# Optimization experiments

Measured on AMD Instinct MI355X. Metric: run time of the kernel, lower is better.

## Reference

```python
import jax, jax.numpy as jnp
import numpy as np

B, M, D = 16, 16, 512          # m (tokens per sample) must equal num_experts
N = 16                          # num_experts
H = (D + D) * 2 // 3            # hidden_dim = 682
OUT = 512


def setup_inputs() -> dict:
    key = jax.random.key(0)
    ks = jax.random.split(key, 8)
    s = lambda k, shape, fan: jax.random.normal(k, shape, jnp.float32) / np.sqrt(fan)
    return {
        "x":    jax.random.normal(ks[0], (B, M, D), jnp.float32),
        "phi":  jax.random.normal(ks[1], (D, N, H), jnp.float32),
        "W1":   s(ks[2], (N, D, H), D),
        "b1":   s(ks[3], (N, H), D),
        "W2":   s(ks[4], (N, H, D), H),
        "b2":   s(ks[5], (N, D), H),
        "Wout": s(ks[6], (N * D, OUT), N * D),
        "bout": s(ks[7], (OUT,), N * D),
    }


def reference(x, phi, W1, b1, W2, b2, Wout, bout):
    # dispatch/combine logits: [b, m, n, p]
    logits = jnp.einsum('bmd,dnp->bmnp', x, phi)
    Dw = jax.nn.softmax(logits, axis=1)                       # dispatch weights over tokens m
    Cw = jax.nn.softmax(jax.nn.softmax(logits, axis=2), axis=3)  # (softmax of softmax, faithful)
    Xs = jnp.einsum('bmd,bmnp->bnpd', x, Dw)                  # expert slot inputs [b,n,p,d]
    # batched per-expert MLP (grouped GEMM over expert axis n)
    hmid = jax.nn.relu(jnp.einsum('bnpd,ndh->bnph', Xs, W1) + b1[None, :, None, :])
    Ys = jnp.einsum('bnph,nhd->bnpd', hmid, W2) + b2[None, :, None, :]
    Y = jnp.einsum('bnpd,bmnp->bmd', Ys, Cw)                  # combine -> [b, m, d]
    flat = Y.reshape(Y.shape[0], -1)                          # [b, m*d] == [b, n*d]
    return flat @ Wout + bout
```

## Files before the change

### kernel.cpp

```cpp
#include <hip/hip_runtime.h>
#include <hip/hip_bf16.h>
#include <math.h>

typedef unsigned int   u32;
typedef unsigned short u16;
typedef __bf16 bf16;
typedef bf16  bf16x8  __attribute__((ext_vector_type(8)));
typedef float f32x4   __attribute__((ext_vector_type(4)));
typedef float f32x16  __attribute__((ext_vector_type(16)));

#define BBATCH 16
#define MTOK   16
#define NEXP   16
#define DDIM   512
#define HDIM   682
#define HPAD   704
#define NHCOL  (NEXP*HDIM)
#define NHPCOL (NEXP*HPAD)

__device__ __forceinline__ u16 f2bf(float f) {
    u32 u = __builtin_bit_cast(u32, f);
    u += 0x7fffu + ((u >> 16) & 1u);
    return (u16)(u >> 16);
}
__device__ __forceinline__ float bf2f(u16 h) {
    u32 u = ((u32)h) << 16;
    return __builtin_bit_cast(float, u);
}
__device__ __forceinline__ u32 pk2bf(float a, float b) {
    __hip_bfloat162 t = __float22bfloat162_rn(float2{a, b});
    u32 r;
    __builtin_memcpy(&r, &t, 4);
    return r;
}

__global__ __launch_bounds__(256) void k_prep(
    const float* __restrict__ x, const float* __restrict__ b2,
    const float* __restrict__ bout,
    u16* __restrict__ xh, u16* __restrict__ xl,
    float* __restrict__ Y, float* __restrict__ out, u16* __restrict__ DwT) {
    const int bid = blockIdx.x, tid = threadIdx.x;
    if (bid < 128) {
        int i = (bid * 256 + tid) * 4;
        float4 v = *(const float4*)&x[i];
        float a[4] = {v.x, v.y, v.z, v.w};
        u16 hh[4], ll[4];
        #pragma unroll
        for (int j = 0; j < 4; ++j) {
            hh[j] = f2bf(a[j]);
            ll[j] = f2bf(a[j] - bf2f(hh[j]));
        }
        *(uint2*)&xh[i] = make_uint2((u32)hh[0] | ((u32)hh[1] << 16), (u32)hh[2] | ((u32)hh[3] << 16));
        *(uint2*)&xl[i] = make_uint2((u32)ll[0] | ((u32)ll[1] << 16), (u32)ll[2] | ((u32)ll[3] << 16));
    } else if (bid < 640) {
        int idx = (bid - 128) * 256 + tid;
        int d = idx & 511;
        float s = 0.f;
        #pragma unroll
        for (int nn = 0; nn < 16; ++nn) s += b2[nn * 512 + d];
        Y[idx] = s;
    } else if (bid < 672) {
        int idx = (bid - 640) * 256 + tid;
        out[idx] = bout[idx & 511];
    } else {
        int g = (bid - 672) * 256 + tid;
        int bn = g / 88, off = g - bn * 88;
        *(uint2*)(DwT + (size_t)(bn * HPAD + HDIM) * 16 + off * 4) = make_uint2(0u, 0u);
    }
}

__global__ __launch_bounds__(256) void k_lt1(
    const u16* __restrict__ xh, const u16* __restrict__ xl,
    const float* __restrict__ phi, const float* __restrict__ W1,
    float* __restrict__ logits, u16* __restrict__ DwT, u16* __restrict__ T1b) {
    __shared__ __align__(16) char SMEM[29184];
    const int bid = blockIdx.x, tid = threadIdx.x;
    const int wv = tid >> 6, lane = tid & 63, quad = lane >> 4, l15 = lane & 15;
    if (bid < 704) {
        const int xcd = bid & 7, slot = bid >> 3;
        const int rt = slot & 3, ct = (slot >> 2) * 8 + xcd;
        if (ct >= 171) return;
        u16* AH = (u16*)SMEM;
        u16* AL = (u16*)(SMEM + 5120);
        u16* BH = (u16*)(SMEM + 10240);
        u16* BL = (u16*)(SMEM + 15360);
        float* F = (float*)(SMEM + 20480);
        const int r = tid >> 2, kg = (tid & 3) * 8;
        const u16* aph = xh + (size_t)(rt * 64 + r) * 512 + kg;
        const u16* apl = xl + (size_t)(rt * 64 + r) * 512 + kg;
        const int dl = tid >> 3, cg = (tid & 7) * 8;
        const int c0 = ct * 64 + cg;
        float vB[8];
        auto loadB = [&](int kb) {
            const float* src = phi + (size_t)(kb + dl) * NHCOL + c0;
            if (c0 + 8 <= NHCOL) {
                *(float4*)&vB[0] = *(const float4*)&src[0];
                *(float4*)&vB[4] = *(const float4*)&src[4];
            } else {
                #pragma unroll
                for (int i = 0; i < 8; ++i) vB[i] = (c0 + i < NHCOL) ? src[i] : 0.f;
            }
        };
        uint4 rAh = *(const uint4*)aph;
        uint4 rAl = *(const uint4*)apl;
        loadB(0);
        f32x4 acc[4] = {};
        for (int kb = 0; kb < 512; kb += 32) {
            *(uint4*)&AH[r * 40 + kg] = rAh;
            *(uint4*)&AL[r * 40 + kg] = rAl;
            *(float4*)&F[dl * 68 + cg]     = *(float4*)&vB[0];
            *(float4*)&F[dl * 68 + cg + 4] = *(float4*)&vB[4];
            __syncthreads();
            if (kb + 32 < 512) {
                rAh = *(const uint4*)(aph + kb + 32);
                rAl = *(const uint4*)(apl + kb + 32);
                loadB(kb + 32);
            }
            {
                int cc = tid & 63, q = tid >> 6;
                u16 th[8], tl[8];
                #pragma unroll
                for (int i = 0; i < 8; ++i) {
                    float v = F[(q * 8 + i) * 68 + cc];
                    th[i] = f2bf(v);
                    tl[i] = f2bf(v - bf2f(th[i]));
                }
                *(uint4*)&BH[cc * 40 + q * 8] = *(uint4*)&th[0];
                *(uint4*)&BL[cc * 40 + q * 8] = *(uint4*)&tl[0];
            }
            __syncthreads();
            bf16x8 ah = *(const bf16x8*)&AH[(wv * 16 + l15) * 40 + quad * 8];
            bf16x8 al = *(const bf16x8*)&AL[(wv * 16 + l15) * 40 + quad * 8];
            #pragma unroll
            for (int j = 0; j < 4; ++j) {
                bf16x8 bh = *(const bf16x8*)&BH[(j * 16 + l15) * 40 + quad * 8];
                bf16x8 bl = *(const bf16x8*)&BL[(j * 16 + l15) * 40 + quad * 8];
                acc[j] = __builtin_amdgcn_mfma_f32_16x16x32_bf16(ah, bh, acc[j], 0, 0, 0);
                acc[j] = __builtin_amdgcn_mfma_f32_16x16x32_bf16(ah, bl, acc[j], 0, 0, 0);
                acc[j] = __builtin_amdgcn_mfma_f32_16x16x32_bf16(al, bh, acc[j], 0, 0, 0);
            }
            __syncthreads();
        }
        const int b  = rt * 4 + wv;
        const int r0 = rt * 64 + wv * 16 + quad * 4;
        #pragma unroll
        for (int j = 0; j < 4; ++j) {
            const int col = ct * 64 + j * 16 + l15;
            float a0 = acc[j][0], a1 = acc[j][1], a2 = acc[j][2], a3 = acc[j][3];
            if (col < NHCOL) {
                logits[(size_t)(r0 + 0) * NHCOL + col] = a0;
                logits[(size_t)(r0 + 1) * NHCOL + col] = a1;
                logits[(size_t)(r0 + 2) * NHCOL + col] = a2;
                logits[(size_t)(r0 + 3) * NHCOL + col] = a3;
            }
            float mx = fmaxf(fmaxf(a0, a1), fmaxf(a2, a3));
            mx = fmaxf(mx, __shfl_xor(mx, 16));
            mx = fmaxf(mx, __shfl_xor(mx, 32));
            float e0 = expf(a0 - mx), e1 = expf(a1 - mx);
            float e2 = expf(a2 - mx), e3 = expf(a3 - mx);
            float s = e0 + e1 + e2 + e3;
            s += __shfl_xor(s, 16);
            s += __shfl_xor(s, 32);
            float inv = 1.f / s;
            if (col < NHCOL) {
                int n = col / HDIM;
                int p = col - n * HDIM;
                u16* dst = DwT + ((size_t)((b * 16 + n) * HPAD + p)) * 16 + quad * 4;
                *(uint2*)dst = make_uint2(pk2bf(e0 * inv, e1 * inv), pk2bf(e2 * inv, e3 * inv));
            }
        }
    } else {
        const int b2_ = bid - 704;
        const int xcd = b2_ & 7, slot = b2_ >> 3;
        const int rh = slot & 1, ct = (slot >> 1) * 8 + xcd;
        const int n = ct / 11, h0 = (ct % 11) * 64;
        u16* As = (u16*)SMEM;
        u16* Bs = (u16*)(SMEM + 10240);
        float* F = (float*)(SMEM + 15360);
        const int r = tid >> 1, kg = (tid & 1) * 16;
        const u16* ap = xh + (size_t)(rh * 128 + r) * 512 + kg;
        const int dl = tid >> 3, cg = (tid & 7) * 8;
        const int h = h0 + cg;
        float vB[8];
        auto loadB = [&](int kb) {
            const float* wr = W1 + ((size_t)n * 512 + kb + dl) * HDIM + h;
            if (h + 8 <= HDIM) {
                #pragma unroll
                for (int i = 0; i < 4; ++i) {
                    float2 t = *(const float2*)&wr[i * 2];
                    vB[i * 2] = t.x; vB[i * 2 + 1] = t.y;
                }
            } else {
                #pragma unroll
                for (int i = 0; i < 8; ++i) vB[i] = (h + i < HDIM) ? wr[i] : 0.f;
            }
        };
        uint4 rA0 = *(const uint4*)ap;
        uint4 rA1 = *(const uint4*)(ap + 8);
        loadB(0);
        f32x4 acc[2][4] = {};
        for (int kb = 0; kb < 512; kb += 32) {
            *(uint4*)&As[r * 40 + kg]     = rA0;
            *(uint4*)&As[r * 40 + kg + 8] = rA1;
            *(float4*)&F[dl * 68 + cg]     = *(float4*)&vB[0];
            *(float4*)&F[dl * 68 + cg + 4] = *(float4*)&vB[4];
            __syncthreads();
            if (kb + 32 < 512) {
                rA0 = *(const uint4*)(ap + kb + 32);
                rA1 = *(const uint4*)(ap + kb + 40);
                loadB(kb + 32);
            }
            {
                int cc = tid & 63, q = tid >> 6;
                u16 tv[8];
                #pragma unroll
                for (int i = 0; i < 8; ++i) tv[i] = f2bf(F[(q * 8 + i) * 68 + cc]);
                *(uint4*)&Bs[cc * 40 + q * 8] = *(uint4*)&tv[0];
            }
            __syncthreads();
            bf16x8 af[2], bfr[4];
            #pragma unroll
            for (int i = 0; i < 2; ++i)
                af[i] = *(const bf16x8*)&As[(wv * 32 + i * 16 + l15) * 40 + quad * 8];
            #pragma unroll
            for (int j = 0; j < 4; ++j)
                bfr[j] = *(const bf16x8*)&Bs[(j * 16 + l15) * 40 + quad * 8];
            #pragma unroll
            for (int i = 0; i < 2; ++i)
                #pragma unroll
                for (int j = 0; j < 4; ++j)
                    acc[i][j] = __builtin_amdgcn_mfma_f32_16x16x32_bf16(af[i], bfr[j], acc[i][j], 0, 0, 0);
            __syncthreads();
        }
        #pragma unroll
        for (int i = 0; i < 2; ++i)
            #pragma unroll
            for (int j = 0; j < 4; ++j) {
                int col = ct * 64 + j * 16 + l15;
                int r0  = rh * 128 + wv * 32 + i * 16 + quad * 4;
                #pragma unroll
                for (int rr = 0; rr < 4; ++rr)
                    T1b[(size_t)(r0 + rr) * NHPCOL + col] = f2bf(acc[i][j][rr]);
            }
    }
}

__global__ __launch_bounds__(256) void k_cw(
    const float* __restrict__ L, u16* __restrict__ CwB) {
    __shared__ float row[NHCOL];
    const int bid = blockIdx.x, tid = threadIdx.x;
    const int m = bid & 15, b = bid >> 4;
    const float* Lrow = L + (size_t)(b * 16 + m) * NHCOL;
    for (int i = tid; i < NHCOL; i += 256) row[i] = Lrow[i];
    __syncthreads();
    for (int p = tid; p < HDIM; p += 256) {
        float v[16];
        float mx = -1e30f;
        #pragma unroll
        for (int n = 0; n < 16; ++n) { v[n] = row[n * HDIM + p]; mx = fmaxf(mx, v[n]); }
        float s = 0.f;
        #pragma unroll
        for (int n = 0; n < 16; ++n) { v[n] = expf(v[n] - mx); s += v[n]; }
        float inv = 1.f / s;
        #pragma unroll
        for (int n = 0; n < 16; ++n) row[n * HDIM + p] = expf(v[n] * inv);
    }
    __syncthreads();
    const int wv = tid >> 6, lane = tid & 63;
    for (int nn = 0; nn < 4; ++nn) {
        int n = wv * 4 + nn;
        float s = 0.f;
        for (int p = lane; p < HDIM; p += 64) s += row[n * HDIM + p];
        #pragma unroll
        for (int off = 32; off > 0; off >>= 1) s += __shfl_xor(s, off);
        float inv = 1.f / s;
        u16* dst = CwB + (size_t)(((b * 16 + n) * 16 + m)) * HPAD;
        for (int p = lane; p < HDIM; p += 64) dst[p] = f2bf(row[n * HDIM + p] * inv);
        if (lane < HPAD - HDIM) dst[HDIM + lane] = 0;
    }
}

__global__ __launch_bounds__(256) void k_mid(
    const u16* __restrict__ T1b, const u16* __restrict__ DwT,
    const u16* __restrict__ CwB, const float* __restrict__ b1,
    u16* __restrict__ Gb) {
    __shared__ u16 T1T[128 * 24];
    __shared__ u16 hmidT[128 * 64];
    const int bid = blockIdx.x;
    const int xcd = bid & 7, slot = bid >> 3;
    const int ht = slot % 6, gg = slot / 6;
    const int g = gg * 8 + xcd;
    const int n = g & 15, b = g >> 4;
    const int tid = threadIdx.x;
    const int wv = tid >> 6, lane = tid & 63;
    const int quad = lane >> 4, l15 = lane & 15;
    const int l31 = lane & 31, half = lane >> 5;
    const int h0 = ht * 128;
    const int b16n = b * 16 + n;

    {
        int m = tid & 15, hh0 = (tid >> 4) * 8;
        u16 v[8];
        if (h0 + hh0 + 8 <= HPAD) {
            *(uint4*)v = *(const uint4*)(T1b + (size_t)(b * 16 + m) * NHPCOL + n * HPAD + h0 + hh0);
        } else {
            #pragma unroll
            for (int i = 0; i < 8; ++i) v[i] = 0;
        }
        #pragma unroll
        for (int i = 0; i < 8; ++i) T1T[(hh0 + i) * 24 + m] = v[i];
    }
    __syncthreads();

    const int hrow = wv * 32 + l31;
    bf16x8 bt1 = *(const bf16x8*)&T1T[hrow * 24 + half * 8];
    int hg1 = h0 + hrow;
    float biasf = (hg1 < HDIM) ? b1[n * HDIM + hg1] : 0.f;
    f32x16 cbias;
    #pragma unroll
    for (int i = 0; i < 16; ++i) cbias[i] = biasf;

    const u16* dwbase = DwT + (size_t)(b16n * HPAD) * 16;
    const u16* cwrow  = CwB + (size_t)(b16n * 16 + l15) * HPAD;

    f32x4 acc[2] = {};
    const int hsw = hrow & 7;
    for (int c = 0; c < 11; ++c) {
        const int p0 = c * 64;
        #pragma unroll
        for (int pt = 0; pt < 2; ++pt) {
            bf16x8 adw = *(const bf16x8*)(dwbase + (size_t)(p0 + pt * 32 + l31) * 16 + half * 8);
            f32x16 hm = __builtin_amdgcn_mfma_f32_32x32x16_bf16(adw, bt1, cbias, 0, 0, 0);
            #pragma unroll
            for (int g2 = 0; g2 < 4; ++g2) {
                float v0 = fmaxf(hm[g2 * 4 + 0], 0.f);
                float v1 = fmaxf(hm[g2 * 4 + 1], 0.f);
                float v2 = fmaxf(hm[g2 * 4 + 2], 0.f);
                float v3 = fmaxf(hm[g2 * 4 + 3], 0.f);
                uint2 pk = make_uint2(pk2bf(v0, v1), pk2bf(v2, v3));
                int gran = (pt * 4 + g2) ^ hsw;
                *(uint2*)&hmidT[hrow * 64 + gran * 8 + half * 4] = pk;
            }
        }
        #pragma unroll
        for (int s = 0; s < 2; ++s) {
            bf16x8 acw = *(const bf16x8*)(cwrow + p0 + s * 32 + quad * 8);
            #pragma unroll
            for (int hj = 0; hj < 2; ++hj) {
                int hr = wv * 32 + hj * 16 + l15;
                int gr = (s * 4 + quad) ^ (hr & 7);
                bf16x8 bh = *(const bf16x8*)&hmidT[hr * 64 + gr * 8];
                acc[hj] = __builtin_amdgcn_mfma_f32_16x16x32_bf16(acw, bh, acc[hj], 0, 0, 0);
            }
        }
    }
    #pragma unroll
    for (int hj = 0; hj < 2; ++hj) {
        int h = h0 + wv * 32 + hj * 16 + l15;
        if (h < HPAD) {
            #pragma unroll
            for (int r = 0; r < 4; ++r) {
                int m = quad * 4 + r;
                Gb[(size_t)(b * 16 + m) * NHPCOL + n * HPAD + h] = f2bf(acc[hj][r]);
            }
        }
    }
}

__global__ __launch_bounds__(256) void k_ygemm(
    const u16* __restrict__ G, const float* __restrict__ W2, float* __restrict__ Y) {
    __shared__ u16 AsL[64 * 40];
    __shared__ u16 BsL[128 * 40];
    __shared__ float F[32 * 132];
    const int bid = blockIdx.x;
    const int xcd = bid & 7, slot = bid >> 3;
    const int rt = slot & 3, gg = slot >> 2;
    const int g = gg * 8 + xcd;
    const int ct = g & 3, nz = g >> 2;
    const int n = nz >> 1, kb0 = (nz & 1) * 352;
    const int tid = threadIdx.x;
    const int wv = tid >> 6, lane = tid & 63, quad = lane >> 4, l15 = lane & 15;
    const int m0 = rt * 64, d0 = ct * 128;
    const int am = tid >> 2, akg = (tid & 3) * 8;
    const u16* apg = G + (size_t)(m0 + am) * NHPCOL + n * HPAD + akg;
    const int hl = tid >> 3, cg = (tid & 7) * 16;
    float vB[16];
    auto loadB = [&](int kb) {
        int h = kb + hl;
        if (h < HDIM) {
            const float* src = W2 + ((size_t)n * HDIM + h) * 512 + d0 + cg;
            *(float4*)&vB[0]  = *(const float4*)&src[0];
            *(float4*)&vB[4]  = *(const float4*)&src[4];
            *(float4*)&vB[8]  = *(const float4*)&src[8];
            *(float4*)&vB[12] = *(const float4*)&src[12];
        } else {
            #pragma unroll
            for (int i = 0; i < 16; ++i) vB[i] = 0.f;
        }
    };
    uint4 rA = *(const uint4*)(apg + kb0);
    loadB(kb0);
    f32x4 acc[4][2] = {};
    for (int kb = kb0; kb < kb0 + 352; kb += 32) {
        *(uint4*)&AsL[am * 40 + akg] = rA;
        *(float4*)&F[hl * 132 + cg]      = *(float4*)&vB[0];
        *(float4*)&F[hl * 132 + cg + 4]  = *(float4*)&vB[4];
        *(float4*)&F[hl * 132 + cg + 8]  = *(float4*)&vB[8];
        *(float4*)&F[hl * 132 + cg + 12] = *(float4*)&vB[12];
        __syncthreads();
        if (kb + 32 < kb0 + 352) {
            rA = *(const uint4*)(apg + kb + 32);
            loadB(kb + 32);
        }
        {
            int cc = tid & 127, half = tid >> 7;
            u16 tv[16];
            #pragma unroll
            for (int i = 0; i < 16; ++i) tv[i] = f2bf(F[(half * 16 + i) * 132 + cc]);
            *(uint4*)&BsL[cc * 40 + half * 16]     = *(uint4*)&tv[0];
            *(uint4*)&BsL[cc * 40 + half * 16 + 8] = *(uint4*)&tv[8];
        }
        __syncthreads();
        bf16x8 af[4], bfr[2];
        #pragma unroll
        for (int i = 0; i < 4; ++i) af[i] = *(const bf16x8*)&AsL[(i * 16 + l15) * 40 + quad * 8];
        #pragma unroll
        for (int j = 0; j < 2; ++j) bfr[j] = *(const bf16x8*)&BsL[(wv * 32 + j * 16 + l15) * 40 + quad * 8];
        #pragma unroll
        for (int i = 0; i < 4; ++i)
            #pragma unroll
            for (int j = 0; j < 2; ++j)
                acc[i][j] = __builtin_amdgcn_mfma_f32_16x16x32_bf16(af[i], bfr[j], acc[i][j], 0, 0, 0);
        __syncthreads();
    }
    #pragma unroll
    for (int i = 0; i < 4; ++i)
        #pragma unroll
        for (int j = 0; j < 2; ++j) {
            int d = d0 + wv * 32 + j * 16 + l15;
            int r0 = m0 + i * 16 + quad * 4;
            #pragma unroll
            for (int r = 0; r < 4; ++r)
                atomicAdd(&Y[(size_t)(r0 + r) * 512 + d], acc[i][j][r]);
        }
}

__global__ __launch_bounds__(256) void k_outgemm(
    const float* __restrict__ Y, const float* __restrict__ Wout, float* __restrict__ out) {
    __shared__ u16 AsL[16 * 40];
    __shared__ u16 BsL[128 * 40];
    __shared__ float F[32 * 132];
    const int ct = blockIdx.x, ks = blockIdx.y;
    const int tid = threadIdx.x;
    const int wv = tid >> 6, lane = tid & 63, quad = lane >> 4, l15 = lane & 15;
    const int o0 = ct * 128, kbase = ks * 64;
    f32x4 acc[2] = {};
    for (int kb = 0; kb < 64; kb += 32) {
        {
            int r = tid >> 4, k2 = (tid & 15) * 2;
            float2 v = *(const float2*)&Y[(size_t)r * 8192 + kbase + kb + k2];
            AsL[r * 40 + k2]     = f2bf(v.x);
            AsL[r * 40 + k2 + 1] = f2bf(v.y);
        }
        {
            int kl = tid >> 3, cg = (tid & 7) * 16;
            const float* src = Wout + (size_t)(kbase + kb + kl) * 512 + o0 + cg;
            float v[16];
            *(float4*)&v[0]  = *(const float4*)&src[0];
            *(float4*)&v[4]  = *(const float4*)&src[4];
            *(float4*)&v[8]  = *(const float4*)&src[8];
            *(float4*)&v[12] = *(const float4*)&src[12];
            #pragma unroll
            for (int i = 0; i < 16; ++i) F[kl * 132 + cg + i] = v[i];
        }
        __syncthreads();
        {
            int cc = tid & 127, half = tid >> 7;
            u16 tv[16];
            #pragma unroll
            for (int i = 0; i < 16; ++i) tv[i] = f2bf(F[(half * 16 + i) * 132 + cc]);
            *(uint4*)&BsL[cc * 40 + half * 16]     = *(uint4*)&tv[0];
            *(uint4*)&BsL[cc * 40 + half * 16 + 8] = *(uint4*)&tv[8];
        }
        __syncthreads();
        bf16x8 af = *(const bf16x8*)&AsL[l15 * 40 + quad * 8];
        #pragma unroll
        for (int j = 0; j < 2; ++j) {
            bf16x8 bfr = *(const bf16x8*)&BsL[(wv * 32 + j * 16 + l15) * 40 + quad * 8];
            acc[j] = __builtin_amdgcn_mfma_f32_16x16x32_bf16(af, bfr, acc[j], 0, 0, 0);
        }
        __syncthreads();
    }
    #pragma unroll
    for (int j = 0; j < 2; ++j) {
        int o = o0 + wv * 32 + j * 16 + l15;
        #pragma unroll
        for (int r = 0; r < 4; ++r)
            atomicAdd(&out[(size_t)(quad * 4 + r) * 512 + o], acc[j][r]);
    }
}

extern "C" void kernel_launch(void* const* d_in, const int* in_sizes, int n_in,
                              void* d_out, int out_size, void* d_ws, size_t ws_size,
                              hipStream_t stream) {
    const float* x    = (const float*)d_in[0];
    const float* phi  = (const float*)d_in[1];
    const float* W1   = (const float*)d_in[2];
    const float* b1   = (const float*)d_in[3];
    const float* W2   = (const float*)d_in[4];
    const float* b2   = (const float*)d_in[5];
    const float* Wout = (const float*)d_in[6];
    const float* bout = (const float*)d_in[7];
    float* out = (float*)d_out;

    char* base = (char*)d_ws;
    float* logits = (float*)(base + 0);
    u16*   DwT    = (u16*)(base + 11173888);
    u16*   CwB    = (u16*)(base + 16941056);
    u16*   T1b    = (u16*)(base + 22708224);
    u16*   Gb     = (u16*)(base + 28475392);
    u16*   xh     = (u16*)(base + 34242560);
    u16*   xl     = (u16*)(base + 34504704);
    float* Y      = (float*)(base + 34766848);

    k_prep    <<<dim3(760), 256, 0, stream>>>(x, b2, bout, xh, xl, Y, out, DwT);
    k_lt1     <<<dim3(1056), 256, 0, stream>>>(xh, xl, phi, W1, logits, DwT, T1b);
    k_cw      <<<dim3(256), 256, 0, stream>>>(logits, CwB);
    k_mid     <<<dim3(1536), 256, 0, stream>>>(T1b, DwT, CwB, b1, Gb);
    k_ygemm   <<<dim3(512), 256, 0, stream>>>(Gb, W2, Y);
    k_outgemm <<<dim3(4, 128), 256, 0, stream>>>(Y, Wout, out);
}
```

Baseline: 216.3 us.

## Double-buffer LDS tiles and load B columns directly to drop fp32 staging

Four GEMM kernels (logits/T1, ygemm, outgemm) now load their fp32 B operand column-wise per thread, converting to bf16 in registers and writing straight into the transposed LDS layout. This removes the fp32 staging buffer and one of the three barriers per k-step. A ping-pong LDS buffer also removes the trailing barrier. The cost is global loads that become scalar, strided along K (still coalesced across threads by column), in place of vector float4 loads.

```diff
diff --git a/kernel.cpp b/kernel.cpp
--- a/kernel.cpp
+++ b/kernel.cpp
@@ -73,73 +73,59 @@
     const u16* __restrict__ xh, const u16* __restrict__ xl,
     const float* __restrict__ phi, const float* __restrict__ W1,
     float* __restrict__ logits, u16* __restrict__ DwT, u16* __restrict__ T1b) {
-    __shared__ __align__(16) char SMEM[29184];
+    __shared__ __align__(16) u16 S[20480];
     const int bid = blockIdx.x, tid = threadIdx.x;
     const int wv = tid >> 6, lane = tid & 63, quad = lane >> 4, l15 = lane & 15;
     if (bid < 704) {
         const int xcd = bid & 7, slot = bid >> 3;
         const int rt = slot & 3, ct = (slot >> 2) * 8 + xcd;
         if (ct >= 171) return;
-        u16* AH = (u16*)SMEM;
-        u16* AL = (u16*)(SMEM + 5120);
-        u16* BH = (u16*)(SMEM + 10240);
-        u16* BL = (u16*)(SMEM + 15360);
-        float* F = (float*)(SMEM + 20480);
         const int r = tid >> 2, kg = (tid & 3) * 8;
         const u16* aph = xh + (size_t)(rt * 64 + r) * 512 + kg;
         const u16* apl = xl + (size_t)(rt * 64 + r) * 512 + kg;
-        const int dl = tid >> 3, cg = (tid & 7) * 8;
-        const int c0 = ct * 64 + cg;
+        const int cc = tid & 63, q8 = (tid >> 6) * 8;
+        const int c = ct * 64 + cc;
         float vB[8];
         auto loadB = [&](int kb) {
-            const float* src = phi + (size_t)(kb + dl) * NHCOL + c0;
-            if (c0 + 8 <= NHCOL) {
-                *(float4*)&vB[0] = *(const float4*)&src[0];
-                *(float4*)&vB[4] = *(const float4*)&src[4];
-            } else {
-                #pragma unroll
-                for (int i = 0; i < 8; ++i) vB[i] = (c0 + i < NHCOL) ? src[i] : 0.f;
-            }
+            const float* src = phi + (size_t)(kb + q8) * NHCOL + c;
+            #pragma unroll
+            for (int i = 0; i < 8; ++i)
+                vB[i] = (c < NHCOL) ? src[(size_t)i * NHCOL] : 0.f;
         };
         uint4 rAh = *(const uint4*)aph;
         uint4 rAl = *(const uint4*)apl;
         loadB(0);
         f32x4 acc[4] = {};
-        for (int kb = 0; kb < 512; kb += 32) {
-            *(uint4*)&AH[r * 40 + kg] = rAh;
-            *(uint4*)&AL[r * 40 + kg] = rAl;
-            *(float4*)&F[dl * 68 + cg]     = *(float4*)&vB[0];
-            *(float4*)&F[dl * 68 + cg + 4] = *(float4*)&vB[4];
+        for (int s = 0; s < 16; ++s) {
+            const int kb = s * 32, p = (s & 1) * 2560;
+            *(uint4*)&S[p + r * 40 + kg]        = rAh;
+            *(uint4*)&S[5120 + p + r * 40 + kg] = rAl;
+            {
+                u16 th[8], tl[8];
+                #pragma unroll
+                for (int i = 0; i < 8; ++i) {
+                    th[i] = f2bf(vB[i]);
+                    tl[i] = f2bf(vB[i] - bf2f(th[i]));
+                }
+                *(uint4*)&S[10240 + p + cc * 40 + q8] = *(uint4*)&th[0];
+                *(uint4*)&S[15360 + p + cc * 40 + q8] = *(uint4*)&tl[0];
+            }
             __syncthreads();
-            if (kb + 32 < 512) {
+            if (s < 15) {
                 rAh = *(const uint4*)(aph + kb + 32);
                 rAl = *(const uint4*)(apl + kb + 32);
                 loadB(kb + 32);
             }
-            {
-                int cc = tid & 63, q = tid >> 6;
-                u16 th[8], tl[8];
-                #pragma unroll
-                for (int i = 0; i < 8; ++i) {
-                    float v = F[(q * 8 + i) * 68 + cc];
-                    th[i] = f2bf(v);
-                    tl[i] = f2bf(v - bf2f(th[i]));
-                }
-                *(uint4*)&BH[cc * 40 + q * 8] = *(uint4*)&th[0];
-                *(uint4*)&BL[cc * 40 + q * 8] = *(uint4*)&tl[0];
-            }
-            __syncthreads();
-            bf16x8 ah = *(const bf16x8*)&AH[(wv * 16 + l15) * 40 + quad * 8];
-            bf16x8 al = *(const bf16x8*)&AL[(wv * 16 + l15) * 40 + quad * 8];
+            bf16x8 ah = *(const bf16x8*)&S[p + (wv * 16 + l15) * 40 + quad * 8];
+            bf16x8 al = *(const bf16x8*)&S[5120 + p + (wv * 16 + l15) * 40 + quad * 8];
             #pragma unroll
             for (int j = 0; j < 4; ++j) {
-                bf16x8 bh = *(const bf16x8*)&BH[(j * 16 + l15) * 40 + quad * 8];
-                bf16x8 bl = *(const bf16x8*)&BL[(j * 16 + l15) * 40 + quad * 8];
+                bf16x8 bh = *(const bf16x8*)&S[10240 + p + (j * 16 + l15) * 40 + quad * 8];
+                bf16x8 bl = *(const bf16x8*)&S[15360 + p + (j * 16 + l15) * 40 + quad * 8];
                 acc[j] = __builtin_amdgcn_mfma_f32_16x16x32_bf16(ah, bh, acc[j], 0, 0, 0);
                 acc[j] = __builtin_amdgcn_mfma_f32_16x16x32_bf16(ah, bl, acc[j], 0, 0, 0);
                 acc[j] = __builtin_amdgcn_mfma_f32_16x16x32_bf16(al, bh, acc[j], 0, 0, 0);
             }
-            __syncthreads();
         }
         const int b  = rt * 4 + wv;
         const int r0 = rt * 64 + wv * 16 + quad * 4;
@@ -164,8 +150,8 @@
             float inv = 1.f / s;
             if (col < NHCOL) {
                 int n = col / HDIM;
-                int p = col - n * HDIM;
-                u16* dst = DwT + ((size_t)((b * 16 + n) * HPAD + p)) * 16 + quad * 4;
+                int p2 = col - n * HDIM;
+                u16* dst = DwT + ((size_t)((b * 16 + n) * HPAD + p2)) * 16 + quad * 4;
                 *(uint2*)dst = make_uint2(pk2bf(e0 * inv, e1 * inv), pk2bf(e2 * inv, e3 * inv));
             }
         }
@@ -174,63 +160,49 @@
         const int xcd = b2_ & 7, slot = b2_ >> 3;
         const int rh = slot & 1, ct = (slot >> 1) * 8 + xcd;
         const int n = ct / 11, h0 = (ct % 11) * 64;
-        u16* As = (u16*)SMEM;
-        u16* Bs = (u16*)(SMEM + 10240);
-        float* F = (float*)(SMEM + 15360);
         const int r = tid >> 1, kg = (tid & 1) * 16;
         const u16* ap = xh + (size_t)(rh * 128 + r) * 512 + kg;
-        const int dl = tid >> 3, cg = (tid & 7) * 8;
-        const int h = h0 + cg;
+        const int cc = tid & 63, q8 = (tid >> 6) * 8;
+        const int h = h0 + cc;
         float vB[8];
         auto loadB = [&](int kb) {
-            const float* wr = W1 + ((size_t)n * 512 + kb + dl) * HDIM + h;
-            if (h + 8 <= HDIM) {
-                #pragma unroll
-                for (int i = 0; i < 4; ++i) {
-                    float2 t = *(const float2*)&wr[i * 2];
-                    vB[i * 2] = t.x; vB[i * 2 + 1] = t.y;
-                }
-            } else {
-                #pragma unroll
-                for (int i = 0; i < 8; ++i) vB[i] = (h + i < HDIM) ? wr[i] : 0.f;
-            }
+            const float* src = W1 + ((size_t)n * 512 + kb + q8) * HDIM + h;
+            #pragma unroll
+            for (int i = 0; i < 8; ++i)
+                vB[i] = (h < HDIM) ? src[(size_t)i * HDIM] : 0.f;
         };
         uint4 rA0 = *(const uint4*)ap;
         uint4 rA1 = *(const uint4*)(ap + 8);
         loadB(0);
         f32x4 acc[2][4] = {};
-        for (int kb = 0; kb < 512; kb += 32) {
-            *(uint4*)&As[r * 40 + kg]     = rA0;
-            *(uint4*)&As[r * 40 + kg + 8] = rA1;
-            *(float4*)&F[dl * 68 + cg]     = *(float4*)&vB[0];
-            *(float4*)&F[dl * 68 + cg + 4] = *(float4*)&vB[4];
+        for (int s = 0; s < 16; ++s) {
+            const int kb = s * 32, pA = (s & 1) * 5120, pB = 10240 + (s & 1) * 2560;
+            *(uint4*)&S[pA + r * 40 + kg]     = rA0;
+            *(uint4*)&S[pA + r * 40 + kg + 8] = rA1;
+            {
+                u16 tv[8];
+                #pragma unroll
+                for (int i = 0; i < 8; ++i) tv[i] = f2bf(vB[i]);
+                *(uint4*)&S[pB + cc * 40 + q8] = *(uint4*)&tv[0];
+            }
             __syncthreads();
-            if (kb + 32 < 512) {
+            if (s < 15) {
                 rA0 = *(const uint4*)(ap + kb + 32);
                 rA1 = *(const uint4*)(ap + kb + 40);
                 loadB(kb + 32);
             }
-            {
-                int cc = tid & 63, q = tid >> 6;
-                u16 tv[8];
-                #pragma unroll
-                for (int i = 0; i < 8; ++i) tv[i] = f2bf(F[(q * 8 + i) * 68 + cc]);
-                *(uint4*)&Bs[cc * 40 + q * 8] = *(uint4*)&tv[0];
-            }
-            __syncthreads();
             bf16x8 af[2], bfr[4];
             #pragma unroll
             for (int i = 0; i < 2; ++i)
-                af[i] = *(const bf16x8*)&As[(wv * 32 + i * 16 + l15) * 40 + quad * 8];
+                af[i] = *(const bf16x8*)&S[pA + (wv * 32 + i * 16 + l15) * 40 + quad * 8];
             #pragma unroll
             for (int j = 0; j < 4; ++j)
-                bfr[j] = *(const bf16x8*)&Bs[(j * 16 + l15) * 40 + quad * 8];
+                bfr[j] = *(const bf16x8*)&S[pB + (j * 16 + l15) * 40 + quad * 8];
             #pragma unroll
             for (int i = 0; i < 2; ++i)
                 #pragma unroll
                 for (int j = 0; j < 4; ++j)
                     acc[i][j] = __builtin_amdgcn_mfma_f32_16x16x32_bf16(af[i], bfr[j], acc[i][j], 0, 0, 0);
-            __syncthreads();
         }
         #pragma unroll
         for (int i = 0; i < 2; ++i)
@@ -369,9 +341,7 @@
 
 __global__ __launch_bounds__(256) void k_ygemm(
     const u16* __restrict__ G, const float* __restrict__ W2, float* __restrict__ Y) {
-    __shared__ u16 AsL[64 * 40];
-    __shared__ u16 BsL[128 * 40];
-    __shared__ float F[32 * 132];
+    __shared__ __align__(16) u16 S[15360];
     const int bid = blockIdx.x;
     const int xcd = bid & 7, slot = bid >> 3;
     const int rt = slot & 3, gg = slot >> 2;
@@ -383,120 +353,106 @@
     const int m0 = rt * 64, d0 = ct * 128;
     const int am = tid >> 2, akg = (tid & 3) * 8;
     const u16* apg = G + (size_t)(m0 + am) * NHPCOL + n * HPAD + akg;
-    const int hl = tid >> 3, cg = (tid & 7) * 16;
+    const int dd = tid & 127, q16 = (tid >> 7) * 16;
+    const int d = d0 + dd;
     float vB[16];
     auto loadB = [&](int kb) {
-        int h = kb + hl;
-        if (h < HDIM) {
-            const float* src = W2 + ((size_t)n * HDIM + h) * 512 + d0 + cg;
-            *(float4*)&vB[0]  = *(const float4*)&src[0];
-            *(float4*)&vB[4]  = *(const float4*)&src[4];
-            *(float4*)&vB[8]  = *(const float4*)&src[8];
-            *(float4*)&vB[12] = *(const float4*)&src[12];
-        } else {
-            #pragma unroll
-            for (int i = 0; i < 16; ++i) vB[i] = 0.f;
+        #pragma unroll
+        for (int i = 0; i < 16; ++i) {
+            int hh = kb + q16 + i;
+            vB[i] = (hh < HDIM) ? W2[((size_t)n * HDIM + hh) * 512 + d] : 0.f;
         }
     };
     uint4 rA = *(const uint4*)(apg + kb0);
     loadB(kb0);
     f32x4 acc[4][2] = {};
-    for (int kb = kb0; kb < kb0 + 352; kb += 32) {
-        *(uint4*)&AsL[am * 40 + akg] = rA;
-        *(float4*)&F[hl * 132 + cg]      = *(float4*)&vB[0];
-        *(float4*)&F[hl * 132 + cg + 4]  = *(float4*)&vB[4];
-        *(float4*)&F[hl * 132 + cg + 8]  = *(float4*)&vB[8];
-        *(float4*)&F[hl * 132 + cg + 12] = *(float4*)&vB[12];
+    for (int s = 0; s < 11; ++s) {
+        const int kb = kb0 + s * 32, pA = (s & 1) * 2560, pB = 5120 + (s & 1) * 5120;
+        *(uint4*)&S[pA + am * 40 + akg] = rA;
+        {
+            u16 tv[16];
+            #pragma unroll
+            for (int i = 0; i < 16; ++i) tv[i] = f2bf(vB[i]);
+            *(uint4*)&S[pB + dd * 40 + q16]     = *(uint4*)&tv[0];
+            *(uint4*)&S[pB + dd * 40 + q16 + 8] = *(uint4*)&tv[8];
+        }
         __syncthreads();
-        if (kb + 32 < kb0 + 352) {
+        if (s < 10) {
             rA = *(const uint4*)(apg + kb + 32);
             loadB(kb + 32);
         }
-        {
-            int cc = tid & 127, half = tid >> 7;
-            u16 tv[16];
-            #pragma unroll
-            for (int i = 0; i < 16; ++i) tv[i] = f2bf(F[(half * 16 + i) * 132 + cc]);
-            *(uint4*)&BsL[cc * 40 + half * 16]     = *(uint4*)&tv[0];
-            *(uint4*)&BsL[cc * 40 + half * 16 + 8] = *(uint4*)&tv[8];
-        }
-        __syncthreads();
         bf16x8 af[4], bfr[2];
         #pragma unroll
-        for (int i = 0; i < 4; ++i) af[i] = *(const bf16x8*)&AsL[(i * 16 + l15) * 40 + quad * 8];
-        #pragma unroll
-        for (int j = 0; j < 2; ++j) bfr[j] = *(const bf16x8*)&BsL[(wv * 32 + j * 16 + l15) * 40 + quad * 8];
+        for (int i = 0; i < 4; ++i) af[i] = *(const bf16x8*)&S[pA + (i * 16 + l15) * 40 + quad * 8];
+        #pragma unroll
+        for (int j = 0; j < 2; ++j) bfr[j] = *(const bf16x8*)&S[pB + (wv * 32 + j * 16 + l15) * 40 + quad * 8];
         #pragma unroll
         for (int i = 0; i < 4; ++i)
             #pragma unroll
             for (int j = 0; j < 2; ++j)
                 acc[i][j] = __builtin_amdgcn_mfma_f32_16x16x32_bf16(af[i], bfr[j], acc[i][j], 0, 0, 0);
-        __syncthreads();
     }
     #pragma unroll
     for (int i = 0; i < 4; ++i)
         #pragma unroll
         for (int j = 0; j < 2; ++j) {
-            int d = d0 + wv * 32 + j * 16 + l15;
+            int dcol = d0 + wv * 32 + j * 16 + l15;
             int r0 = m0 + i * 16 + quad * 4;
             #pragma unroll
             for (int r = 0; r < 4; ++r)
-                atomicAdd(&Y[(size_t)(r0 + r) * 512 + d], acc[i][j][r]);
+                atomicAdd(&Y[(size_t)(r0 + r) * 512 + dcol], acc[i][j][r]);
         }
 }
 
 __global__ __launch_bounds__(256) void k_outgemm(
     const float* __restrict__ Y, const float* __restrict__ Wout, float* __restrict__ out) {
-    __shared__ u16 AsL[16 * 40];
-    __shared__ u16 BsL[128 * 40];
-    __shared__ float F[32 * 132];
+    __shared__ __align__(16) u16 S[11520];
     const int ct = blockIdx.x, ks = blockIdx.y;
     const int tid = threadIdx.x;
     const int wv = tid >> 6, lane = tid & 63, quad = lane >> 4, l15 = lane & 15;
     const int o0 = ct * 128, kbase = ks * 64;
+    const int r_ = tid >> 4, k2 = (tid & 15) * 2;
+    const float* ypg = Y + (size_t)r_ * 8192 + kbase + k2;
+    const int dd = tid & 127, q16 = (tid >> 7) * 16;
+    const int o = o0 + dd;
+    float vB[16];
+    auto loadB = [&](int kb) {
+        #pragma unroll
+        for (int i = 0; i < 16; ++i)
+            vB[i] = Wout[(size_t)(kbase + kb + q16 + i) * 512 + o];
+    };
+    float2 ya = *(const float2*)ypg;
+    loadB(0);
     f32x4 acc[2] = {};
-    for (int kb = 0; kb < 64; kb += 32) {
+    for (int s = 0; s < 2; ++s) {
+        const int kb = s * 32, pA = (s & 1) * 640, pB = 1280 + (s & 1) * 5120;
+        S[pA + r_ * 40 + k2]     = f2bf(ya.x);
+        S[pA + r_ * 40 + k2 + 1] = f2bf(ya.y);
         {
-            int r = tid >> 4, k2 = (tid & 15) * 2;
-            float2 v = *(const float2*)&Y[(size_t)r * 8192 + kbase + kb + k2];
-            AsL[r * 40 + k2]     = f2bf(v.x);
-            AsL[r * 40 + k2 + 1] = f2bf(v.y);
-        }
-        {
-            int kl = tid >> 3, cg = (tid & 7) * 16;
-            const float* src = Wout + (size_t)(kbase + kb + kl) * 512 + o0 + cg;
-            float v[16];
-            *(float4*)&v[0]  = *(const float4*)&src[0];
-            *(float4*)&v[4]  = *(const float4*)&src[4];
-            *(float4*)&v[8]  = *(const float4*)&src[8];
-            *(float4*)&v[12] = *(const float4*)&src[12];
-            #pragma unroll
-            for (int i = 0; i < 16; ++i) F[kl * 132 + cg + i] = v[i];
+            u16 tv[16];
+            #pragma unroll
+            for (int i = 0; i < 16; ++i) tv[i] = f2bf(vB[i]);
+            *(uint4*)&S[pB + dd * 40 + q16]     = *(uint4*)&tv[0];
+            *(uint4*)&S[pB + dd * 40 + q16 + 8] = *(uint4*)&tv[8];
         }
         __syncthreads();
-        {
-            int cc = tid & 127, half = tid >> 7;
-            u16 tv[16];
-            #pragma unroll
-            for (int i = 0; i < 16; ++i) tv[i] = f2bf(F[(half * 16 + i) * 132 + cc]);
-            *(uint4*)&BsL[cc * 40 + half * 16]     = *(uint4*)&tv[0];
-            *(uint4*)&BsL[cc * 40 + half * 16 + 8] = *(uint4*)&tv[8];
-        }
-        __syncthreads();
-        bf16x8 af = *(const bf16x8*)&AsL[l15 * 40 + quad * 8];
+        if (s < 1) {
+            ya = *(const float2*)(ypg + kb + 32);
+            loadB(kb + 32);
+        }
+        bf16x8 af = *(const bf16x8*)&S[pA + l15 * 40 + quad * 8];
         #pragma unroll
         for (int j = 0; j < 2; ++j) {
-            bf16x8 bfr = *(const bf16x8*)&BsL[(wv * 32 + j * 16 + l15) * 40 + quad * 8];
+            bf16x8 bfr = *(const bf16x8*)&S[pB + (wv * 32 + j * 16 + l15) * 40 + quad * 8];
             acc[j] = __builtin_amdgcn_mfma_f32_16x16x32_bf16(af, bfr, acc[j], 0, 0, 0);
         }
-        __syncthreads();
     }
     #pragma unroll
     for (int j = 0; j < 2; ++j) {
-        int o = o0 + wv * 32 + j * 16 + l15;
+        int oc = o0 + wv * 32 + j * 16 + l15;
         #pragma unroll
         for (int r = 0; r < 4; ++r)
-            atomicAdd(&out[(size_t)(quad * 4 + r) * 512 + o], acc[j][r]);
+            atomicAdd(&out[(size_t)(quad * 4 + r) * 512 + oc], acc[j][r]);
     }
 }
 
```

New measurement: 220.0 us. No clear change (+1.7%).
